# Kernel optimization log

Measured on AMD Instinct MI355X. Metric: run time of the kernel, lower is better.

## Reference

```python
import jax, jax.numpy as jnp
import numpy as np

B, S, D_IN = 4, 2048, 1024
H, D_HEAD = 16, 64  # num_head, num_out; H*D_HEAD == D_IN here
LN_EPS = 1e-5


def setup_inputs() -> dict:
    key = jax.random.key(0)
    ks = jax.random.split(key, 5)
    scale = 1.0 / np.sqrt(D_IN)
    return {
        "x": jax.random.normal(ks[0], (B, S, D_IN), dtype=jnp.float32),
        "Wq": jax.random.normal(ks[1], (H * D_HEAD, D_IN), dtype=jnp.float32) * scale,
        "Wk": jax.random.normal(ks[2], (H * D_HEAD, D_IN), dtype=jnp.float32) * scale,
        "Wv": jax.random.normal(ks[3], (H * D_HEAD, D_IN), dtype=jnp.float32) * scale,
        "Wr": jax.random.normal(ks[4], (H * D_HEAD, D_IN), dtype=jnp.float32) * scale,
        "gamma": jnp.ones((H * D_HEAD,), dtype=jnp.float32),
        "beta": jnp.zeros((H * D_HEAD,), dtype=jnp.float32),
    }


def reference(x, Wq, Wk, Wv, Wr, gamma, beta):
    b, s, _ = x.shape
    # Linear (no bias), torch weight layout [out, in]; split heads head-major
    q = (x @ Wq.T).reshape(b, s, H, D_HEAD)
    k = (x @ Wk.T).reshape(b, s, H, D_HEAD)
    v = (x @ Wv.T).reshape(b, s, H, D_HEAD)
    # full O(S^2) score matrix, as in the original
    scores = jnp.einsum("bqhd,bkhd->bhqk", q, k) / jnp.sqrt(jnp.float32(D_HEAD))
    weights = jax.nn.softmax(scores, axis=-1)
    attn = jnp.einsum("bhqk,bkhd->bqhd", weights, v).reshape(b, s, H * D_HEAD)
    out = jax.nn.relu(attn + x @ Wr.T)
    # LayerNorm over last dim with affine params
    mu = jnp.mean(out, axis=-1, keepdims=True)
    var = jnp.mean(jnp.square(out - mu), axis=-1, keepdims=True)
    out = (out - mu) * jax.lax.rsqrt(var + LN_EPS) * gamma + beta
    return out
```

## Files before the change

kernel.cpp:

```cpp
#include <hip/hip_runtime.h>
#include <hip/hip_bf16.h>
#include <stdint.h>

constexpr int BB = 4;
constexpr int SS = 2048;
constexpr int DIN = 1024;
constexpr int HH = 16;
constexpr int DH = 64;
constexpr int NOUT = 4096;
constexpr int MROWS = BB * SS;

typedef __attribute__((ext_vector_type(8))) short bf16x8;
typedef __attribute__((ext_vector_type(8))) unsigned short u16x8;
typedef __attribute__((ext_vector_type(4))) unsigned short u16x4;
typedef __attribute__((ext_vector_type(4))) float f32x4;

__device__ __forceinline__ unsigned short f2bf(float f) {
  unsigned int x = __float_as_uint(f);
  unsigned int r = (x + 0x7fffu + ((x >> 16) & 1u)) >> 16;
  return (unsigned short)r;
}
__device__ __forceinline__ float bf2f(unsigned short u) {
  return __uint_as_float(((unsigned int)u) << 16);
}

__device__ __forceinline__ void gload16(const void* g, void* l) {
  typedef __attribute__((address_space(1))) void gvoid;
  typedef __attribute__((address_space(3))) void lvoid;
  __builtin_amdgcn_global_load_lds((gvoid*)(uintptr_t)g, (lvoid*)l, 16, 0, 0);
}

__global__ __launch_bounds__(256) void convert_x(const float* __restrict__ src,
                                                 unsigned short* __restrict__ dst) {
  int i = (blockIdx.x * 256 + threadIdx.x) * 8;
  f32x4 a = *(const f32x4*)(src + i);
  f32x4 b = *(const f32x4*)(src + i + 4);
  u16x8 o;
  o[0] = f2bf(a[0]); o[1] = f2bf(a[1]); o[2] = f2bf(a[2]); o[3] = f2bf(a[3]);
  o[4] = f2bf(b[0]); o[5] = f2bf(b[1]); o[6] = f2bf(b[2]); o[7] = f2bf(b[3]);
  *(u16x8*)(dst + i) = o;
}

__global__ __launch_bounds__(256) void convert_w(const float* __restrict__ Wq,
                                                 const float* __restrict__ Wk,
                                                 const float* __restrict__ Wv,
                                                 const float* __restrict__ Wr,
                                                 unsigned short* __restrict__ dst) {
  int i = (blockIdx.x * 256 + threadIdx.x) * 8;
  int seg = i >> 20;
  const float* src = (seg == 0) ? Wq : (seg == 1) ? Wk : (seg == 2) ? Wv : Wr;
  float scale = (seg == 0) ? 0.125f * 1.44269504088896f : 1.0f;
  int j = i & 1048575;
  f32x4 a = *(const f32x4*)(src + j);
  f32x4 b = *(const f32x4*)(src + j + 4);
  u16x8 o;
  o[0] = f2bf(a[0] * scale); o[1] = f2bf(a[1] * scale);
  o[2] = f2bf(a[2] * scale); o[3] = f2bf(a[3] * scale);
  o[4] = f2bf(b[0] * scale); o[5] = f2bf(b[1] * scale);
  o[6] = f2bf(b[2] * scale); o[7] = f2bf(b[3] * scale);
  *(u16x8*)(dst + i) = o;
}

constexpr int GBM = 128, GBN = 128, GBK = 64;

__global__ __launch_bounds__(256) void gemm_qkvr(const unsigned short* __restrict__ X,
                                                 const unsigned short* __restrict__ Wt,
                                                 unsigned short* __restrict__ Y) {
  const int K = DIN;
  const int nbn = NOUT / GBN;
  int bid = blockIdx.x;
  int idx = (bid & 7) * 256 + (bid >> 3);
  int bm = idx / nbn, bn = idx % nbn;
  int m0 = bm * GBM, n0 = bn * GBN;
  int t = threadIdx.x;
  int w = t >> 6, l = t & 63;
  int lg = l >> 4, ll = l & 15;
  int wm = (w >> 1) * 64, wn = (w & 1) * 64;

  __shared__ unsigned short As[2][GBM * GBK];
  __shared__ unsigned short Bs[2][GBN * GBK];

  f32x4 acc[4][4];
#pragma unroll
  for (int i = 0; i < 4; i++)
#pragma unroll
    for (int j = 0; j < 4; j++) acc[i][j] = (f32x4)0.0f;

  int grow = t >> 3;
  int gslot = t & 7;

  auto stage = [&](int kt, int bi) {
    int k0 = kt * GBK;
#pragma unroll
    for (int c = 0; c < 4; ++c) {
      int row = c * 32 + grow;
      int col = (gslot ^ (row & 7)) * 8;
      gload16(X + (size_t)(m0 + row) * K + k0 + col, &As[bi][c * 2048 + w * 512]);
      gload16(Wt + (size_t)(n0 + row) * K + k0 + col, &Bs[bi][c * 2048 + w * 512]);
    }
  };

  stage(0, 0);
  stage(1, 1);
  asm volatile("s_waitcnt vmcnt(8)" ::: "memory");
  __builtin_amdgcn_s_barrier();

  for (int kt = 0; kt < 16; ++kt) {
    int cur = kt & 1;
    bf16x8 af[4][2], bfr[4][2];
#pragma unroll
    for (int mt = 0; mt < 4; ++mt)
#pragma unroll
      for (int kk = 0; kk < 2; ++kk) {
        af[mt][kk] = *(const bf16x8*)&As[cur][(wm + mt * 16 + ll) * GBK +
                                             ((kk * 4 + lg) ^ (ll & 7)) * 8];
        bfr[mt][kk] = *(const bf16x8*)&Bs[cur][(wn + mt * 16 + ll) * GBK +
                                              ((kk * 4 + lg) ^ (ll & 7)) * 8];
      }
    __builtin_amdgcn_s_setprio(1);
#pragma unroll
    for (int mt = 0; mt < 4; ++mt)
#pragma unroll
      for (int nt = 0; nt < 4; ++nt)
#pragma unroll
        for (int kk = 0; kk < 2; ++kk)
          acc[mt][nt] = __builtin_amdgcn_mfma_f32_16x16x32_bf16(af[mt][kk], bfr[nt][kk],
                                                                acc[mt][nt], 0, 0, 0);
    __builtin_amdgcn_s_setprio(0);

    asm volatile("s_waitcnt lgkmcnt(0)" ::: "memory");
    __builtin_amdgcn_s_barrier();

    stage((kt + 2) & 15, cur);

    asm volatile("s_waitcnt vmcnt(8)" ::: "memory");
    __builtin_amdgcn_s_barrier();
  }
  asm volatile("s_waitcnt vmcnt(0)" ::: "memory");

#pragma unroll
  for (int mt = 0; mt < 4; ++mt)
#pragma unroll
    for (int nt = 0; nt < 4; ++nt) {
      int n = n0 + wn + nt * 16 + ll;
#pragma unroll
      for (int r = 0; r < 4; ++r) {
        int m = m0 + wm + mt * 16 + lg * 4 + r;
        Y[(size_t)m * NOUT + n] = f2bf(acc[mt][nt][r]);
      }
    }
}

__global__ __launch_bounds__(256) void transpose_v(const unsigned short* __restrict__ qkvr,
                                                   unsigned short* __restrict__ vt) {
  int bh = blockIdx.x >> 5;
  int st = blockIdx.x & 31;
  int b = bh >> 4, h = bh & 15;
  __shared__ unsigned short tile[64][72];
  int t = threadIdx.x;
#pragma unroll
  for (int c = 0; c < 2; ++c) {
    int chunk = t + c * 256;
    int row = chunk >> 3;
    int col = (chunk & 7) * 8;
    u16x8 v = *(const u16x8*)(qkvr + (size_t)(b * SS + st * 64 + row) * NOUT + 2048 + h * DH + col);
    *(u16x8*)&tile[row][col] = v;
  }
  __syncthreads();
  int d = t >> 2;
  int s0 = (t & 3) * 16;
  u16x8 o0, o1;
#pragma unroll
  for (int i = 0; i < 8; ++i) o0[i] = tile[s0 + i][d];
#pragma unroll
  for (int i = 0; i < 8; ++i) o1[i] = tile[s0 + 8 + i][d];
  size_t orow = (size_t)(bh * DH + d) * SS + st * 64 + s0;
  *(u16x8*)(vt + orow) = o0;
  *(u16x8*)(vt + orow + 8) = o1;
}

__global__ __launch_bounds__(512) void attention(const unsigned short* __restrict__ qkvr,
                                                 const unsigned short* __restrict__ vt,
                                                 unsigned short* __restrict__ attn) {
  int bid = blockIdx.x;
  int idx = (bid & 7) * 64 + (bid >> 3);
  int qt = idx & 7;
  int bh = idx >> 3;
  int b = bh >> 4, h = bh & 15;
  int t = threadIdx.x, w = t >> 6, l = t & 63;
  int lg = l >> 4, ll = l & 15;

  __shared__ unsigned short Ks[2][4096];
  __shared__ unsigned short Vs[2][4096];
  __shared__ unsigned short Ps[8][2048];

  const unsigned short* kbase = qkvr + (size_t)(b * SS) * NOUT + 1024 + h * DH;
  const unsigned short* vbase = vt + (size_t)(bh * DH) * SS;

  bf16x8 qb[2][2];
#pragma unroll
  for (int m = 0; m < 2; ++m) {
    int qrow = b * SS + qt * 256 + w * 32 + m * 16 + ll;
#pragma unroll
    for (int kk = 0; kk < 2; ++kk)
      qb[m][kk] = *(const bf16x8*)(qkvr + (size_t)qrow * NOUT + h * DH + kk * 32 + lg * 8);
  }

  bf16x8 ones;
#pragma unroll
  for (int i = 0; i < 8; i++) ones[i] = (short)0x3F80;

  f32x4 acc[2][4];
  f32x4 dacc[2];
#pragma unroll
  for (int m = 0; m < 2; ++m) {
    dacc[m] = (f32x4)0.0f;
#pragma unroll
    for (int i = 0; i < 4; i++) acc[m][i] = (f32x4)0.0f;
  }

  int grow = t >> 3;
  int gcol = ((t & 7) ^ (grow & 7)) * 8;

  auto stage = [&](int tile, int bi) {
    gload16(kbase + (size_t)(tile * 64 + grow) * NOUT + gcol, &Ks[bi][w * 512]);
    gload16(vbase + (size_t)grow * SS + tile * 64 + gcol, &Vs[bi][w * 512]);
  };

  stage(0, 0);

  for (int kt = 0; kt < 32; ++kt) {
    int bi = kt & 1;
    stage((kt + 1) & 31, bi ^ 1);
    asm volatile("s_waitcnt vmcnt(2)" ::: "memory");
    __builtin_amdgcn_s_barrier();
    __builtin_amdgcn_sched_barrier(0);

    f32x4 s[2][4];
#pragma unroll
    for (int m = 0; m < 2; ++m)
#pragma unroll
      for (int nt = 0; nt < 4; nt++) s[m][nt] = (f32x4)0.0f;
    __builtin_amdgcn_s_setprio(1);
#pragma unroll
    for (int nt = 0; nt < 4; ++nt)
#pragma unroll
      for (int kk = 0; kk < 2; ++kk) {
        bf16x8 kb = *(const bf16x8*)&Ks[bi][(nt * 16 + ll) * 64 + ((kk * 4 + lg) ^ (ll & 7)) * 8];
        s[0][nt] = __builtin_amdgcn_mfma_f32_16x16x32_bf16(kb, qb[0][kk], s[0][nt], 0, 0, 0);
        s[1][nt] = __builtin_amdgcn_mfma_f32_16x16x32_bf16(kb, qb[1][kk], s[1][nt], 0, 0, 0);
      }
    __builtin_amdgcn_s_setprio(0);

#pragma unroll
    for (int m = 0; m < 2; ++m)
#pragma unroll
      for (int nt = 0; nt < 4; nt++)
#pragma unroll
        for (int r = 0; r < 4; r++) {
          float e;
          asm("v_exp_f32 %0, %1" : "=v"(e) : "v"(s[m][nt][r]));
          s[m][nt][r] = e;
        }

#pragma unroll
    for (int m = 0; m < 2; ++m) {
      char* prow = (char*)&Ps[w][0] + (m * 16 + ll) * 128;
#pragma unroll
      for (int nt = 0; nt < 4; nt++) {
        unsigned sp0, sp1;
        asm("v_cvt_pk_bf16_f32 %0, %1, %2" : "=v"(sp0) : "v"(s[m][nt][0]), "v"(s[m][nt][1]));
        asm("v_cvt_pk_bf16_f32 %0, %1, %2" : "=v"(sp1) : "v"(s[m][nt][2]), "v"(s[m][nt][3]));
        uint2 pv; pv.x = sp0; pv.y = sp1;
        *(uint2*)(prow + ((2 * nt + (lg >> 1)) ^ (ll & 7)) * 16 + (lg & 1) * 8) = pv;
      }
    }

    bf16x8 pa[2][2];
#pragma unroll
    for (int m = 0; m < 2; ++m)
#pragma unroll
      for (int kk = 0; kk < 2; ++kk)
        pa[m][kk] = *(const bf16x8*)((char*)&Ps[w][0] + (m * 16 + ll) * 128 +
                                     ((4 * kk + lg) ^ (ll & 7)) * 16);

    __builtin_amdgcn_s_setprio(1);
#pragma unroll
    for (int kk = 0; kk < 2; ++kk) {
#pragma unroll
      for (int dt = 0; dt < 4; ++dt) {
        bf16x8 vb = *(const bf16x8*)&Vs[bi][(dt * 16 + ll) * 64 + ((kk * 4 + lg) ^ (ll & 7)) * 8];
        acc[0][dt] = __builtin_amdgcn_mfma_f32_16x16x32_bf16(pa[0][kk], vb, acc[0][dt], 0, 0, 0);
        acc[1][dt] = __builtin_amdgcn_mfma_f32_16x16x32_bf16(pa[1][kk], vb, acc[1][dt], 0, 0, 0);
      }
      dacc[0] = __builtin_amdgcn_mfma_f32_16x16x32_bf16(pa[0][kk], ones, dacc[0], 0, 0, 0);
      dacc[1] = __builtin_amdgcn_mfma_f32_16x16x32_bf16(pa[1][kk], ones, dacc[1], 0, 0, 0);
    }
    __builtin_amdgcn_s_setprio(0);
    __builtin_amdgcn_s_barrier();
    __builtin_amdgcn_sched_barrier(0);
  }
  asm volatile("s_waitcnt vmcnt(0)" ::: "memory");

#pragma unroll
  for (int m = 0; m < 2; ++m)
#pragma unroll
    for (int r = 0; r < 4; r++) {
      float inv = 1.0f / dacc[m][r];
      int arow = b * SS + qt * 256 + w * 32 + m * 16 + lg * 4 + r;
#pragma unroll
      for (int dt = 0; dt < 4; dt++)
        attn[(size_t)arow * DIN + h * DH + dt * 16 + ll] = f2bf(acc[m][dt][r] * inv);
    }
}

__global__ __launch_bounds__(256) void ln_epilogue(const unsigned short* __restrict__ attn,
                                                   const unsigned short* __restrict__ qkvr,
                                                   const float* __restrict__ gamma,
                                                   const float* __restrict__ beta,
                                                   float* __restrict__ out) {
  int row = blockIdx.x;
  int t = threadIdx.x;
  u16x4 av = *(const u16x4*)(attn + (size_t)row * DIN + t * 4);
  u16x4 rv = *(const u16x4*)(qkvr + (size_t)row * NOUT + 3072 + t * 4);
  float v[4];
  float s = 0.0f, s2 = 0.0f;
#pragma unroll
  for (int i = 0; i < 4; i++) {
    v[i] = fmaxf(bf2f(av[i]) + bf2f(rv[i]), 0.0f);
    s += v[i];
    s2 += v[i] * v[i];
  }
#pragma unroll
  for (int m = 1; m < 64; m <<= 1) {
    s += __shfl_xor(s, m);
    s2 += __shfl_xor(s2, m);
  }
  __shared__ float red[2][4];
  int w = t >> 6, l = t & 63;
  if (l == 0) { red[0][w] = s; red[1][w] = s2; }
  __syncthreads();
  s = red[0][0] + red[0][1] + red[0][2] + red[0][3];
  s2 = red[1][0] + red[1][1] + red[1][2] + red[1][3];
  float mu = s * (1.0f / 1024.0f);
  float var = s2 * (1.0f / 1024.0f) - mu * mu;
  float rstd = rsqrtf(var + 1e-5f);
  f32x4 g = *(const f32x4*)(gamma + t * 4);
  f32x4 be = *(const f32x4*)(beta + t * 4);
  f32x4 o;
#pragma unroll
  for (int i = 0; i < 4; i++) o[i] = (v[i] - mu) * rstd * g[i] + be[i];
  *(f32x4*)(out + (size_t)row * DIN + t * 4) = o;
}

extern "C" void kernel_launch(void* const* d_in, const int* in_sizes, int n_in,
                              void* d_out, int out_size, void* d_ws, size_t ws_size,
                              hipStream_t stream) {
  const float* x = (const float*)d_in[0];
  const float* Wq = (const float*)d_in[1];
  const float* Wk = (const float*)d_in[2];
  const float* Wv = (const float*)d_in[3];
  const float* Wr = (const float*)d_in[4];
  const float* gamma = (const float*)d_in[5];
  const float* beta = (const float*)d_in[6];
  float* out = (float*)d_out;

  char* ws = (char*)d_ws;
  unsigned short* x_bf = (unsigned short*)ws;
  unsigned short* w_bf = (unsigned short*)(ws + (16ull << 20));
  unsigned short* qkvr = (unsigned short*)(ws + (24ull << 20));
  unsigned short* vt   = (unsigned short*)(ws + (88ull << 20));
  unsigned short* attn = (unsigned short*)(ws + (104ull << 20));

  convert_x<<<4096, 256, 0, stream>>>(x, x_bf);
  convert_w<<<2048, 256, 0, stream>>>(Wq, Wk, Wv, Wr, w_bf);
  gemm_qkvr<<<(MROWS / GBM) * (NOUT / GBN), 256, 0, stream>>>(x_bf, w_bf, qkvr);
  transpose_v<<<2048, 256, 0, stream>>>(qkvr, vt);
  attention<<<512, 512, 0, stream>>>(qkvr, vt, attn);
  ln_epilogue<<<MROWS, 256, 0, stream>>>(attn, qkvr, gamma, beta, out);
}
```

Baseline: 191.4 us.

## Restructure QKVR GEMM to 256x256 tiles with 8 warps and triple-buffered LDS

The projection GEMM moves from 128x128x64 tiles with 4 warps and double buffering to 256x256x32 tiles with 8 warps and a three-stage LDS ring. Global loads for A and B are split across the two halves of each k-step so they overlap with MFMA work, and LDS uses a new swizzle. The larger tile cuts global and LDS traffic per FLOP. In exchange it raises register pressure (32 accumulators per thread) and leaves only 512 blocks, which may limit occupancy and tail balance.

Result: faster. 184.2 us (-3.8%).

```diff
diff --git a/kernel.cpp b/kernel.cpp
--- a/kernel.cpp
+++ b/kernel.cpp
@@ -61,91 +61,105 @@
   *(u16x8*)(dst + i) = o;
 }
 
-constexpr int GBM = 128, GBN = 128, GBK = 64;
-
-__global__ __launch_bounds__(256) void gemm_qkvr(const unsigned short* __restrict__ X,
+constexpr int GBM = 256, GBN = 256, GBK = 32;
+
+__global__ __launch_bounds__(512) void gemm_qkvr(const unsigned short* __restrict__ X,
                                                  const unsigned short* __restrict__ Wt,
                                                  unsigned short* __restrict__ Y) {
   const int K = DIN;
-  const int nbn = NOUT / GBN;
   int bid = blockIdx.x;
-  int idx = (bid & 7) * 256 + (bid >> 3);
-  int bm = idx / nbn, bn = idx % nbn;
+  int idx = (bid & 7) * 64 + (bid >> 3);
+  int bm = idx >> 4, bn = idx & 15;
   int m0 = bm * GBM, n0 = bn * GBN;
   int t = threadIdx.x;
   int w = t >> 6, l = t & 63;
   int lg = l >> 4, ll = l & 15;
-  int wm = (w >> 1) * 64, wn = (w & 1) * 64;
-
-  __shared__ unsigned short As[2][GBM * GBK];
-  __shared__ unsigned short Bs[2][GBN * GBK];
-
-  f32x4 acc[4][4];
-#pragma unroll
-  for (int i = 0; i < 4; i++)
+  int wr = w & 1, wc = w >> 1;
+
+  __shared__ unsigned short As[3][8192];
+  __shared__ unsigned short Bs[3][8192];
+
+  f32x4 acc[8][4];
+#pragma unroll
+  for (int i = 0; i < 8; i++)
 #pragma unroll
     for (int j = 0; j < 4; j++) acc[i][j] = (f32x4)0.0f;
 
-  int grow = t >> 3;
-  int gslot = t & 7;
-
-  auto stage = [&](int kt, int bi) {
-    int k0 = kt * GBK;
-#pragma unroll
-    for (int c = 0; c < 4; ++c) {
-      int row = c * 32 + grow;
-      int col = (gslot ^ (row & 7)) * 8;
-      gload16(X + (size_t)(m0 + row) * K + k0 + col, &As[bi][c * 2048 + w * 512]);
-      gload16(Wt + (size_t)(n0 + row) * K + k0 + col, &Bs[bi][c * 2048 + w * 512]);
-    }
+  int qA = ((ll & 1) * 4 + lg) ^ ((ll >> 1) & 7);
+  int aoff = (wr * 64 + (ll >> 1)) * 64 + qA * 8;
+  int boff = (wc * 32 + (ll >> 1)) * 64 + qA * 8;
+
+  int qs = (t & 7) ^ ((t >> 3) & 7);
+  int mloc0 = ((t >> 3) << 1) + ((qs >> 2) & 1);
+  int kloc = (qs & 3) * 8;
+
+  auto stageA = [&](int kt, int bi) {
+#pragma unroll
+    for (int c = 0; c < 2; ++c)
+      gload16(X + (size_t)(m0 + mloc0 + c * 128) * K + kt * GBK + kloc,
+              &As[bi][c * 4096 + t * 8]);
   };
-
-  stage(0, 0);
-  stage(1, 1);
-  asm volatile("s_waitcnt vmcnt(8)" ::: "memory");
+  auto stageB = [&](int kt, int bi) {
+#pragma unroll
+    for (int c = 0; c < 2; ++c)
+      gload16(Wt + (size_t)(n0 + mloc0 + c * 128) * K + kt * GBK + kloc,
+              &Bs[bi][c * 4096 + t * 8]);
+  };
+
+  stageA(0, 0); stageB(0, 0);
+  stageA(1, 1); stageB(1, 1);
+  asm volatile("s_waitcnt vmcnt(4)" ::: "memory");
   __builtin_amdgcn_s_barrier();
 
-  for (int kt = 0; kt < 16; ++kt) {
-    int cur = kt & 1;
-    bf16x8 af[4][2], bfr[4][2];
+  int cur = 0;
+  for (int kt = 0; kt < 32; ++kt) {
+    int nb2 = cur + 2; if (nb2 >= 3) nb2 -= 3;
+    int ktp2 = (kt + 2) & 31;
+
+    bf16x8 a[8], b[4];
+#pragma unroll
+    for (int mt = 0; mt < 4; ++mt) a[mt] = *(const bf16x8*)&As[cur][aoff + mt * 512];
+#pragma unroll
+    for (int nt = 0; nt < 4; ++nt) b[nt] = *(const bf16x8*)&Bs[cur][boff + nt * 512];
+    stageA(ktp2, nb2);
+    __builtin_amdgcn_s_barrier();
+    asm volatile("s_waitcnt lgkmcnt(0)" ::: "memory");
+    __builtin_amdgcn_s_setprio(1);
 #pragma unroll
     for (int mt = 0; mt < 4; ++mt)
 #pragma unroll
-      for (int kk = 0; kk < 2; ++kk) {
-        af[mt][kk] = *(const bf16x8*)&As[cur][(wm + mt * 16 + ll) * GBK +
-                                             ((kk * 4 + lg) ^ (ll & 7)) * 8];
-        bfr[mt][kk] = *(const bf16x8*)&Bs[cur][(wn + mt * 16 + ll) * GBK +
-                                              ((kk * 4 + lg) ^ (ll & 7)) * 8];
-      }
+      for (int nt = 0; nt < 4; ++nt)
+        acc[mt][nt] = __builtin_amdgcn_mfma_f32_16x16x32_bf16(a[mt], b[nt], acc[mt][nt], 0, 0, 0);
+    __builtin_amdgcn_s_setprio(0);
+    __builtin_amdgcn_s_barrier();
+
+#pragma unroll
+    for (int mt = 4; mt < 8; ++mt) a[mt] = *(const bf16x8*)&As[cur][aoff + mt * 512];
+    stageB(ktp2, nb2);
+    __builtin_amdgcn_s_barrier();
+    asm volatile("s_waitcnt lgkmcnt(0)" ::: "memory");
     __builtin_amdgcn_s_setprio(1);
 #pragma unroll
-    for (int mt = 0; mt < 4; ++mt)
+    for (int mt = 4; mt < 8; ++mt)
 #pragma unroll
       for (int nt = 0; nt < 4; ++nt)
-#pragma unroll
-        for (int kk = 0; kk < 2; ++kk)
-          acc[mt][nt] = __builtin_amdgcn_mfma_f32_16x16x32_bf16(af[mt][kk], bfr[nt][kk],
-                                                                acc[mt][nt], 0, 0, 0);
+        acc[mt][nt] = __builtin_amdgcn_mfma_f32_16x16x32_bf16(a[mt], b[nt], acc[mt][nt], 0, 0, 0);
     __builtin_amdgcn_s_setprio(0);
-
-    asm volatile("s_waitcnt lgkmcnt(0)" ::: "memory");
-    __builtin_amdgcn_s_barrier();
-
-    stage((kt + 2) & 15, cur);
-
-    asm volatile("s_waitcnt vmcnt(8)" ::: "memory");
-    __builtin_amdgcn_s_barrier();
+    asm volatile("s_waitcnt vmcnt(4)" ::: "memory");
+    __builtin_amdgcn_s_barrier();
+
+    cur += 1; if (cur == 3) cur = 0;
   }
   asm volatile("s_waitcnt vmcnt(0)" ::: "memory");
 
 #pragma unroll
-  for (int mt = 0; mt < 4; ++mt)
+  for (int mt = 0; mt < 8; ++mt)
 #pragma unroll
     for (int nt = 0; nt < 4; ++nt) {
-      int n = n0 + wn + nt * 16 + ll;
+      int n = n0 + wc * 64 + nt * 16 + ll;
 #pragma unroll
       for (int r = 0; r < 4; ++r) {
-        int m = m0 + wm + mt * 16 + lg * 4 + r;
+        int m = m0 + wr * 128 + mt * 16 + lg * 4 + r;
         Y[(size_t)m * NOUT + n] = f2bf(acc[mt][nt][r]);
       }
     }
@@ -374,7 +388,7 @@
 
   convert_x<<<4096, 256, 0, stream>>>(x, x_bf);
   convert_w<<<2048, 256, 0, stream>>>(Wq, Wk, Wv, Wr, w_bf);
-  gemm_qkvr<<<(MROWS / GBM) * (NOUT / GBN), 256, 0, stream>>>(x_bf, w_bf, qkvr);
+  gemm_qkvr<<<(MROWS / GBM) * (NOUT / GBN), 512, 0, stream>>>(x_bf, w_bf, qkvr);
   transpose_v<<<2048, 256, 0, stream>>>(qkvr, vt);
   attention<<<512, 512, 0, stream>>>(qkvr, vt, attn);
   ln_epilogue<<<MROWS, 256, 0, stream>>>(attn, qkvr, gamma, beta, out);
```
